# Optimization experiments

Hardware: AMD Instinct MI355X
Metric: run time of the kernel (lower is better)

Reference implementation:

```python
import jax, jax.numpy as jnp
import numpy as np

NG = 64  # number of graphs in the batch (global_add_pool output rows)

def _bn(x, g, b):
    # BatchNorm1d, training-mode batch statistics over dim 0
    mu = x.mean(0)
    var = x.var(0)
    return (x - mu) * jax.lax.rsqrt(var + 1e-5) * g + b

def _ln(x, g, b):
    mu = x.mean(-1, keepdims=True)
    var = x.var(-1, keepdims=True)
    return (x - mu) * jax.lax.rsqrt(var + 1e-5) * g + b

def _gine(x, ei, ea, eps, w1, b1, w2, b2, n):
    # GINEConv: mlp((1+eps)*x + sum_dst ReLU(x[src] + ea))
    msg = jax.nn.relu(x[ei[0]] + ea)
    agg = jax.ops.segment_sum(msg, ei[1], num_segments=n)
    h = (1.0 + eps) * x + agg
    return jax.nn.relu(h @ w1 + b1) @ w2 + b2

def setup_inputs() -> dict:
    key = jax.random.key(0)
    H, L, RW = 128, 4, 16
    Nn, m, kk = 4096, 2, 32
    S = Nn * m; SK = S * kk
    Ei, Eg = 1048576, 65536
    Vatom, Vbond = 128, 16
    ks = jax.random.split(key, 24)
    f = lambda i, shape: jax.random.normal(ks[i], shape, jnp.float32) * 0.02
    # intra edges sampled within each subgraph block to honor locality
    subs = jax.random.randint(ks[11], (Ei,), 0, S)
    src = subs * kk + jax.random.randint(ks[12], (Ei,), 0, kk)
    dst = subs * kk + jax.random.randint(ks[13], (Ei,), 0, kk)
    inp = {
        "atom_emb": f(0, (Vatom, H)), "bond_emb": f(1, (Vbond, H)),
        "rwse_w": f(2, (RW, H)), "rwse_b": jnp.zeros((H,), jnp.float32),
        "rwse": jax.random.uniform(ks[3], (Nn, RW), jnp.float32),
        "l_eps": jnp.zeros((L,), jnp.float32),
        "l_w1": f(4, (L, H, H)), "l_b1": jnp.zeros((L, H), jnp.float32),
        "l_w2": f(5, (L, H, H)), "l_b2": jnp.zeros((L, H), jnp.float32),
        "l_bng": jnp.ones((L, H), jnp.float32), "l_bnb": jnp.zeros((L, H), jnp.float32),
        "g_eps": jnp.zeros((L,), jnp.float32),
        "g_w1": f(6, (L, H, H)), "g_b1": jnp.zeros((L, H), jnp.float32),
        "g_w2": f(7, (L, H, H)), "g_b2": jnp.zeros((L, H), jnp.float32),
        "g_bng": jnp.ones((L, H), jnp.float32), "g_bnb": jnp.zeros((L, H), jnp.float32),
        "bcast_w": f(8, (L, H, H)),
        "cat_w1": f(9, (L, 2 * H, H)), "cat_b1": jnp.zeros((L, H), jnp.float32),
        "cat_w2": f(10, (L, H, H)), "cat_b2": jnp.zeros((L, H), jnp.float32),
        "ln_g": jnp.ones((L, H), jnp.float32), "ln_b": jnp.zeros((L, H), jnp.float32),
        "x_ids": jax.random.randint(ks[14], (SK,), 0, Vatom),
        "intra_ei": jnp.stack([src, dst]),
        "intra_ea_ids": jax.random.randint(ks[15], (Ei,), 0, Vbond),
        "global_ei": jax.random.randint(ks[16], (2, Eg), 0, Nn),
        "global_ea_ids": jax.random.randint(ks[17], (Eg,), 0, Vbond),
        "node_ids": jax.random.randint(ks[18], (SK,), 0, Nn),
        "valid": jax.random.randint(ks[19], (SK,), 0, 2),
        "batch": jnp.sort(jax.random.randint(ks[20], (Nn,), 0, NG)),
        "k": 32,
    }
    return inp

def reference(atom_emb, bond_emb, rwse_w, rwse_b, rwse, l_eps, l_w1, l_b1, l_w2, l_b2, l_bng, l_bnb, g_eps, g_w1, g_b1, g_w2, g_b2, g_bng, g_bnb, bcast_w, cat_w1, cat_b1, cat_w2, cat_b2, ln_g, ln_b, x_ids, intra_ei, intra_ea_ids, global_ei, global_ea_ids, node_ids, valid, batch, k):
    SK = x_ids.shape[0]; Nn = rwse.shape[0]
    S = SK // k; m = S // Nn
    H = atom_emb.shape[1]; L = l_eps.shape[0]
    ea_flat = bond_emb[intra_ea_ids]          # [Ei, H]
    g_ea = bond_emb[global_ea_ids]            # [Eg, H]
    valid_f = valid.astype(jnp.float32)[:, None]
    h = (atom_emb[x_ids] + jax.nn.relu(rwse @ rwse_w + rwse_b)[node_ids]) * valid_f  # [SK, H]
    node_assign = jnp.repeat(jnp.arange(Nn), m)   # [S]
    root_idx = jnp.arange(S) * k                  # subgraph roots in flat layout
    for i in range(L):
        h_in = h
        h_local = _bn(jax.nn.relu(_gine(h, intra_ei, ea_flat, l_eps[i], l_w1[i], l_b1[i], l_w2[i], l_b2[i], SK)), l_bng[i], l_bnb[i])
        # scatter-mean of root reps onto original nodes (each node has exactly m subgraphs)
        h_node = jax.ops.segment_sum(h[root_idx], node_assign, num_segments=Nn) / m
        h_cross = _bn(jax.nn.relu(_gine(h_node, global_ei, g_ea, g_eps[i], g_w1[i], g_b1[i], g_w2[i], g_b2[i], Nn)), g_bng[i], g_bnb[i])
        h_node = h_node + h_cross
        # broadcast projected node reps back to every flat subgraph position
        h_b = jnp.repeat((h_node @ bcast_w[i])[node_assign], k, axis=0)  # [SK, H]
        h_cat = jnp.concatenate([h_local, h_b], axis=-1)
        h_new = _ln(jax.nn.gelu(h_cat @ cat_w1[i] + cat_b1[i], approximate=False) @ cat_w2[i] + cat_b2[i], ln_g[i], ln_b[i])
        h = (h_in + h_new) * valid_f
    # per-subgraph masked mean (h is already zero at invalid rows)
    cnt = valid_f.reshape(S, k, 1).sum(1)
    h_sub = h.reshape(S, k, H).sum(1) / jnp.maximum(cnt, 1.0)   # [S, H]
    h_nodef = h_sub.reshape(Nn, m, H).mean(1)                   # [Nn, H]
    return jax.ops.segment_sum(h_nodef, batch, num_segments=NG) # [NG, H]
```

## Files before the change

kernel.cpp:

```cpp
#include <hip/hip_runtime.h>
#include <hip/hip_bf16.h>

#define H 128
#define HH 16384
#define LNUM 4
#define NN 4096
#define SS 8192
#define SKK 262144
#define EI 1048576
#define EG 65536
#define NGRAPH 64

typedef unsigned short u16;
typedef unsigned int u32;
typedef __attribute__((ext_vector_type(8))) short s16x8;
typedef __attribute__((ext_vector_type(4))) float f32x4;

__device__ __forceinline__ float b2f(u32 u){ return __uint_as_float(u<<16); }
__device__ __forceinline__ u16 f2b(float f){
  union { __hip_bfloat16 b; u16 u; } x;
  x.b=__float2bfloat16(f);
  return x.u;
}
__device__ __forceinline__ void unp8(uint4 v, float* f){
  f[0]=b2f(v.x&0xFFFF); f[1]=b2f(v.x>>16);
  f[2]=b2f(v.y&0xFFFF); f[3]=b2f(v.y>>16);
  f[4]=b2f(v.z&0xFFFF); f[5]=b2f(v.z>>16);
  f[6]=b2f(v.w&0xFFFF); f[7]=b2f(v.w>>16);
}
__device__ __forceinline__ void unp4(uint2 v, float* f){
  f[0]=b2f(v.x&0xFFFF); f[1]=b2f(v.x>>16);
  f[2]=b2f(v.y&0xFFFF); f[3]=b2f(v.y>>16);
}
__device__ __forceinline__ uint4 pk8(const float* f){
  uint4 r;
  r.x=(u32)f2b(f[0])|((u32)f2b(f[1])<<16);
  r.y=(u32)f2b(f[2])|((u32)f2b(f[3])<<16);
  r.z=(u32)f2b(f[4])|((u32)f2b(f[5])<<16);
  r.w=(u32)f2b(f[6])|((u32)f2b(f[7])<<16);
  return r;
}
__device__ __forceinline__ uint2 pk4(const float* f){
  uint2 r;
  r.x=(u32)f2b(f[0])|((u32)f2b(f[1])<<16);
  r.y=(u32)f2b(f[2])|((u32)f2b(f[3])<<16);
  return r;
}

struct CvtArgs {
  const void* p[26];
  int start[27];
};
struct TransArgs { int src[28]; };

__global__ void k_sniff(const u16* __restrict__ a, int* __restrict__ flag){
  __shared__ int cnt;
  if(threadIdx.x==0) cnt=0;
  __syncthreads();
  int big=0;
  for(int i=threadIdx.x;i<2048;i+=256){
    int e=(a[i]>>7)&0xFF;
    if(e>=127) big++;
  }
  atomicAdd(&cnt,big);
  __syncthreads();
  if(threadIdx.x==0) *flag=(cnt<16)?1:0;
}

__global__ void k_convert(CvtArgs args, const int* __restrict__ flag, float* __restrict__ dst){
  int fl=*flag;
  int total=args.start[26];
  for(int i=blockIdx.x*blockDim.x+threadIdx.x;i<total;i+=gridDim.x*blockDim.x){
    int a=0;
    while(args.start[a+1]<=i) a++;
    int j=i-args.start[a];
    float v;
    if(fl) v=b2f(((const u16*)args.p[a])[j]);
    else   v=((const float*)args.p[a])[j];
    dst[i]=v;
  }
}

__global__ __launch_bounds__(256) void k_trans(const float* __restrict__ par, TransArgs ta, u16* __restrict__ wt){
  const float* s=par+ta.src[blockIdx.x];
  u16* d=wt+(size_t)blockIdx.x*HH;
  for(int i=threadIdx.x;i<HH;i+=256){
    int j=i&7, lane=(i>>3)&63, fc=i>>9;
    int n=fc>>2, kc=fc&3, lr=lane&15, lk=lane>>4;
    int outc=n*16+lr, k=kc*32+lk*8+j;
    d[i]=f2b(s[(size_t)k*H+outc]);
  }
}

__global__ void k_cvtbond(const float* __restrict__ b, u16* __restrict__ bb){
  int i=blockIdx.x*blockDim.x+threadIdx.x;
  if(i<16*H) bb[i]=f2b(b[i]);
}

__global__ __launch_bounds__(128) void k_prepw3(const float* __restrict__ w, const float* __restrict__ cb1,
                        const float* __restrict__ stl, const float* __restrict__ gl, const float* __restrict__ bl,
                        u16* __restrict__ wt3p, float* __restrict__ bias3){
  __shared__ float red[128];
  int c=blockIdx.x, k=threadIdx.x;
  float mu=stl[k]*(1.f/262144.f);
  float var=stl[128+k]*(1.f/262144.f)-mu*mu;
  float s=gl[k]*rsqrtf(var+1e-5f);
  float tt=bl[k]-mu*s;
  float wv=w[(size_t)k*H+c];
  int idx=(((c>>4)*4+(k>>5))*64+((k>>3)&3)*16+(c&15))*8+(k&7);
  wt3p[idx]=f2b(s*wv);
  red[k]=tt*wv;
  __syncthreads();
  for(int d=64;d>0;d>>=1){ if(k<d) red[k]+=red[k+d]; __syncthreads(); }
  if(k==0) bias3[c]=cb1[c]+red[0];
}

__global__ void k_hist(const int* __restrict__ idx, int n, int shift, int* __restrict__ cnt){
  for(int i=blockIdx.x*blockDim.x+threadIdx.x;i<n;i+=gridDim.x*blockDim.x)
    atomicAdd(&cnt[idx[i]>>shift],1);
}

__global__ void k_scan(const int* __restrict__ cnt, int* __restrict__ off, int nbins){
  __shared__ int ts[1024];
  int t=threadIdx.x;
  int per=nbins>>10;
  int base=t*per;
  int s=0;
  for(int j=0;j<per;j++) s+=cnt[base+j];
  ts[t]=s;
  __syncthreads();
  for(int d=1;d<1024;d<<=1){
    int v=(t>=d)?ts[t-d]:0;
    __syncthreads();
    ts[t]+=v;
    __syncthreads();
  }
  int ex=(t==0)?0:ts[t-1];
  for(int j=0;j<per;j++){ off[base+j]=ex; ex+=cnt[base+j]; }
}

__global__ void k_scatter_i(const int* __restrict__ ei, const int* __restrict__ ea,
                            const int* __restrict__ off, int* __restrict__ cur, int* __restrict__ pack){
  for(int i=blockIdx.x*blockDim.x+threadIdx.x;i<EI;i+=gridDim.x*blockDim.x){
    int s=ei[i], d=ei[EI+i];
    int sub=d>>5;
    int pos=off[sub]+atomicAdd(&cur[sub],1);
    pack[pos]=((s&31)<<9)|((d&31)<<4)|(ea[i]&15);
  }
}

__global__ __launch_bounds__(128) void k_sortsub(const int* __restrict__ eoff, const int* __restrict__ ecnt,
                                                 int* __restrict__ epack, int* __restrict__ dstoff){
  __shared__ int ein[512];
  __shared__ int eout[512];
  __shared__ int bcnt[32];
  __shared__ int bpos[32];
  int sub=blockIdx.x, t=threadIdx.x;
  int o=eoff[sub];
  int n=ecnt[sub]; if(n>512) n=512;
  for(int i=t;i<n;i+=128) ein[i]=epack[o+i];
  if(t<32) bcnt[t]=0;
  __syncthreads();
  for(int i=t;i<n;i+=128) atomicAdd(&bcnt[(ein[i]>>4)&31],1);
  __syncthreads();
  if(t==0){
    int s=0;
    for(int b=0;b<32;b++){ bpos[b]=s; s+=bcnt[b]; }
  }
  __syncthreads();
  if(t<32) dstoff[sub*32+t]=bpos[t];
  __syncthreads();
  for(int i=t;i<n;i+=128){
    int p=ein[i];
    int pos=atomicAdd(&bpos[(p>>4)&31],1);
    eout[pos]=p;
  }
  __syncthreads();
  for(int i=t;i<n;i+=128) epack[o+i]=eout[i];
}

__global__ void k_scatter_g(const int* __restrict__ ei, const int* __restrict__ ea,
                            const int* __restrict__ off, int* __restrict__ cur, int* __restrict__ pack){
  for(int i=blockIdx.x*blockDim.x+threadIdx.x;i<EG;i+=gridDim.x*blockDim.x){
    int s=ei[i], d=ei[EG+i];
    int pos=off[d]+atomicAdd(&cur[d],1);
    pack[pos]=(s<<4)|(ea[i]&15);
  }
}

__global__ __launch_bounds__(128) void k_rwse(const float* __restrict__ rwse, const float* __restrict__ w,
                      const float* __restrict__ b, float* __restrict__ rf){
  __shared__ float ws[16*128];
  __shared__ float rv[16];
  int n=blockIdx.x, c=threadIdx.x;
  for(int i=c;i<2048;i+=128) ws[i]=w[i];
  if(c<16) rv[c]=rwse[n*16+c];
  __syncthreads();
  float acc=b[c];
  for(int j=0;j<16;j++) acc=fmaf(rv[j],ws[j*128+c],acc);
  rf[(size_t)n*H+c]=fmaxf(acc,0.f);
}

__global__ void k_h0(const float* __restrict__ atom, const float* __restrict__ rf,
                     const int* __restrict__ xids, const int* __restrict__ nids,
                     const int* __restrict__ valid, u16* __restrict__ h){
  int i=blockIdx.x*blockDim.x+threadIdx.x;
  if(i>=SKK*16) return;
  int r=i>>4, q=i&15;
  const float4* ap=(const float4*)(atom+(size_t)xids[r]*H)+q*2;
  const float4* bp=(const float4*)(rf+(size_t)nids[r]*H)+q*2;
  float4 a0=ap[0],a1=ap[1],b0=bp[0],b1=bp[1];
  float vm=valid[r]?1.f:0.f;
  float f[8]={(a0.x+b0.x)*vm,(a0.y+b0.y)*vm,(a0.z+b0.z)*vm,(a0.w+b0.w)*vm,
              (a1.x+b1.x)*vm,(a1.y+b1.y)*vm,(a1.z+b1.z)*vm,(a1.w+b1.w)*vm};
  ((uint4*)h)[i]=pk8(f);
}

template<int TAIL>
__global__ __launch_bounds__(256,4) void k_fused1(
    const u16* __restrict__ h, const u16* __restrict__ beb,
    const int* __restrict__ eoff, const int* __restrict__ ecnt, const int* __restrict__ epack,
    const int* __restrict__ dstoff,
    const float* __restrict__ epsp, int layer,
    const u16* __restrict__ W1p, const float* __restrict__ b1,
    const u16* __restrict__ W2p, const float* __restrict__ b2,
    u16* __restrict__ Xg, float* __restrict__ stats,
    const u16* __restrict__ W3p, const float* __restrict__ bias3,
    const u16* __restrict__ bbv,
    const u16* __restrict__ Wc2p, const float* __restrict__ cb2,
    const float* __restrict__ lng, const float* __restrict__ lnb,
    const int* __restrict__ validv, u16* __restrict__ hio)
{
  __shared__ u16 hs[64*128];
  __shared__ u16 agx[64*128];
  __shared__ u16 bes[16*128];
  __shared__ u16 epku[2][512];
  __shared__ int doff[2][32];
  float* sst=(float*)&epku[0][0];

  int t=threadIdx.x;
  int grp=t>>7, c=t&127;
  size_t hbase=(size_t)blockIdx.x*64*H;
  int wave=t>>6, lane=t&63, lr=lane&15, lk=lane>>4;
  int rl=wave*16+lr;
  u32 rsw=((u32)(rl&7))<<4;
  int row0=blockIdx.x*64;

  {
    u32 row=(u32)(t>>4), colb=(u32)((t&15)*16);
    *(uint4*)((char*)bes+row*256+(colb^((row&7)<<4)))=((const uint4*)beb)[t];
  }
  int sub=blockIdx.x*2+grp;
  int n=min(ecnt[sub],512);
  int o=eoff[sub];
  if(c<32) doff[grp][c]=dstoff[sub*32+c];
  for(int i=c;i<n;i+=128) epku[grp][i]=(u16)epack[o+i];

  if(TAIL){
    f32x4 a1t[8];
    #pragma unroll
    for(int n8=0;n8<8;n8++) a1t[n8]=(f32x4){0.f,0.f,0.f,0.f};
    const s16x8* B0=(const s16x8*)(Xg+(size_t)(row0+rl)*H);
    #pragma unroll
    for(int kc=0;kc<4;kc++){
      s16x8 bf=B0[kc*4+lk];
      #pragma unroll
      for(int n8=0;n8<8;n8++){
        s16x8 af=*(const s16x8*)(W3p+((n8*4+kc)<<9)+lane*8);
        a1t[n8]=__builtin_amdgcn_mfma_f32_16x16x32_bf16(af,bf,a1t[n8],0,0,0);
      }
    }
    #pragma unroll
    for(int n8=0;n8<8;n8++){
      int c0=n8*16+lk*4;
      float4 b4=*(const float4*)(bias3+c0);
      float rb[4];
      unp4(*(const uint2*)(bbv+(size_t)blockIdx.x*H+c0),rb);
      float vb[4]={b4.x,b4.y,b4.z,b4.w};
      float v[4];
      #pragma unroll
      for(int j=0;j<4;j++){
        float x=a1t[n8][j]+vb[j]+rb[j];
        v[j]=0.5f*x*(1.f+erff(x*0.70710678118654752f));
      }
      *(uint2*)((char*)agx+(u32)rl*256+(((u32)(2*c0))^rsw))=pk4(v);
    }
    f32x4 a2t[8];
    #pragma unroll
    for(int n8=0;n8<8;n8++) a2t[n8]=(f32x4){0.f,0.f,0.f,0.f};
    #pragma unroll
    for(int kc=0;kc<4;kc++){
      u32 cb=(u32)((kc*32+lk*8)*2);
      s16x8 bf=*(const s16x8*)((char*)agx+(u32)rl*256+(cb^rsw));
      #pragma unroll
      for(int n8=0;n8<8;n8++){
        s16x8 af=*(const s16x8*)(Wc2p+((n8*4+kc)<<9)+lane*8);
        a2t[n8]=__builtin_amdgcn_mfma_f32_16x16x32_bf16(af,bf,a2t[n8],0,0,0);
      }
    }
    {
      float s=0.f,q=0.f;
      #pragma unroll
      for(int n8=0;n8<8;n8++){
        int c0=n8*16+lk*4;
        float4 b4=*(const float4*)(cb2+c0);
        float vb[4]={b4.x,b4.y,b4.z,b4.w};
        #pragma unroll
        for(int j=0;j<4;j++){
          float v=a2t[n8][j]+vb[j];
          a2t[n8][j]=v;
          s+=v; q+=v*v;
        }
      }
      s+=__shfl_xor(s,16); s+=__shfl_xor(s,32);
      q+=__shfl_xor(q,16); q+=__shfl_xor(q,32);
      float mu=s*(1.f/128.f);
      float rsig=rsqrtf(q*(1.f/128.f)-mu*mu+1e-5f);
      #pragma unroll
      for(int n8=0;n8<8;n8++){
        int c0=n8*16+lk*4;
        float4 g4=*(const float4*)(lng+c0);
        float4 e4=*(const float4*)(lnb+c0);
        float g[4]={g4.x,g4.y,g4.z,g4.w}, e[4]={e4.x,e4.y,e4.z,e4.w};
        float ov[4];
        #pragma unroll
        for(int j=0;j<4;j++) ov[j]=(a2t[n8][j]-mu)*rsig*g[j]+e[j];
        *(uint2*)((char*)agx+(u32)rl*256+(((u32)(2*c0))^rsw))=pk4(ov);
      }
    }
    __syncthreads();
    uint4* hp=(uint4*)(hio+hbase);
    #pragma unroll
    for(int p=0;p<4;p++){
      int i=t+p*256;
      u32 row=(u32)(i>>4), colb=(u32)((i&15)*16);
      int grow=row0+(int)row;
      uint4 v=*(const uint4*)((const char*)agx+row*256+(colb^((row&7)<<4)));
      uint4 r=hp[i];
      float vv[8],rv[8],o8[8];
      unp8(v,vv); unp8(r,rv);
      float vm=validv[grow]?1.f:0.f;
      #pragma unroll
      for(int j=0;j<8;j++) o8[j]=(rv[j]+vv[j])*vm;
      uint4 pk=pk8(o8);
      hp[i]=pk;
      *(uint4*)((char*)hs+row*256+(colb^((row&7)<<4)))=pk;
    }
  } else {
    const uint4* src=(const uint4*)(h+hbase);
    #pragma unroll
    for(int i0=0;i0<4;i0++){
      int i=t+i0*256;
      u32 row=(u32)(i>>4), colb=(u32)((i&15)*16);
      *(uint4*)((char*)hs+row*256+(colb^((row&7)<<4)))=src[i];
    }
  }
  __syncthreads();

  {
    float ep=1.f+epsp[layer];
    #pragma unroll
    for(int p=0;p<4;p++){
      int i=t+p*256;
      u32 row=(u32)(i>>4), colb=(u32)((i&15)*16);
      u32 off=row*256+(colb^((row&7)<<4));
      float hf[8],o8[8];
      unp8(*(const uint4*)((const char*)hs+off),hf);
      #pragma unroll
      for(int j=0;j<8;j++) o8[j]=ep*hf[j];
      *(uint4*)((char*)agx+off)=pk8(o8);
    }
  }
  __syncthreads();

  {
    int slot=c>>4, chg=c&15;
    u32 cbyte=(u32)chg*16;
    int d0=slot*4;
    int sA=doff[grp][d0],   eAs=doff[grp][d0+1];
    int sB=doff[grp][d0+1], eBs=doff[grp][d0+2];
    int sC=doff[grp][d0+2], eCs=doff[grp][d0+3];
    int sD=doff[grp][d0+3];
    int eDs=(d0+3==31)?n:doff[grp][d0+4];
    int c1=eAs-sA;
    int c2=c1+eBs-sB;
    int c3=c2+eCs-sC;
    int tot=c3+eDs-sD;
    const u16* ep_=&epku[grp][0];
    auto VIDX=[&](int j)->int{
      return (j<c1)? sA+j : (j<c2)? sB+j-c1 : (j<c3)? sC+j-c2 : sD+j-c3;
    };
    auto LDP=[&](int p, uint4& hv, uint4& bv){
      u32 srow=(u32)(grp*32+(p>>9));
      u32 erow=(u32)(p&15);
      hv=*(const uint4*)((const char*)hs+srow*256+(cbyte^((srow&7)<<4)));
      bv=*(const uint4*)((const char*)bes+erow*256+(cbyte^((erow&7)<<4)));
    };
    int pA=0,pBv=0,pP0=0,pP1=0;
    uint4 hvA,bvA,hvB,bvB;
    hvA=bvA=hvB=bvB=make_uint4(0,0,0,0);
    if(tot>0){ pA=ep_[VIDX(0)]; LDP(pA,hvA,bvA); }
    if(tot>1){ pBv=ep_[VIDX(1)]; LDP(pBv,hvB,bvB); }
    pP0=(tot>2)?ep_[VIDX(2)]:0;
    pP1=(tot>3)?ep_[VIDX(3)]:0;
    float acc[8]={0.f,0.f,0.f,0.f,0.f,0.f,0.f,0.f};
    int cur=-1;
    int j=0;
    while(j<tot){
      {
        float hf[8],bf8[8];
        unp8(hvA,hf); unp8(bvA,bf8);
        int pc=pA;
        if(j+2<tot){ pA=pP0; LDP(pA,hvA,bvA); }
        pP0=pP1;
        pP1=ep_[(j+4<tot)?VIDX(j+4):0];
        int dl=(pc>>4)&31;
        if(dl!=cur){
          if(cur>=0){
            u32 drow=(u32)(grp*32+cur);
            u32 aoff=drow*256+(cbyte^((drow&7)<<4));
            float of[8];
            unp8(*(const uint4*)((const char*)agx+aoff),of);
            #pragma unroll
            for(int q=0;q<8;q++) of[q]+=acc[q];
            *(uint4*)((char*)agx+aoff)=pk8(of);
          }
          #pragma unroll
          for(int q=0;q<8;q++) acc[q]=0.f;
          cur=dl;
        }
        #pragma unroll
        for(int q=0;q<8;q++) acc[q]+=fmaxf(hf[q]+bf8[q],0.f);
      }
      j++;
      if(j>=tot) break;
      {
        float hf[8],bf8[8];
        unp8(hvB,hf); unp8(bvB,bf8);
        int pc=pBv;
        if(j+2<tot){ pBv=pP0; LDP(pBv,hvB,bvB); }
        pP0=pP1;
        pP1=ep_[(j+4<tot)?VIDX(j+4):0];
        int dl=(pc>>4)&31;
        if(dl!=cur){
          if(cur>=0){
            u32 drow=(u32)(grp*32+cur);
            u32 aoff=drow*256+(cbyte^((drow&7)<<4));
            float of[8];
            unp8(*(const uint4*)((const char*)agx+aoff),of);
            #pragma unroll
            for(int q=0;q<8;q++) of[q]+=acc[q];
            *(uint4*)((char*)agx+aoff)=pk8(of);
          }
          #pragma unroll
          for(int q=0;q<8;q++) acc[q]=0.f;
          cur=dl;
        }
        #pragma unroll
        for(int q=0;q<8;q++) acc[q]+=fmaxf(hf[q]+bf8[q],0.f);
      }
      j++;
    }
    if(cur>=0){
      u32 drow=(u32)(grp*32+cur);
      u32 aoff=drow*256+(cbyte^((drow&7)<<4));
      float of[8];
      unp8(*(const uint4*)((const char*)agx+aoff),of);
      #pragma unroll
      for(int q=0;q<8;q++) of[q]+=acc[q];
      *(uint4*)((char*)agx+aoff)=pk8(of);
    }
  }
  __syncthreads();
  sst[t]=0.f;
  __syncthreads();

  f32x4 a1[8];
  #pragma unroll
  for(int n8=0;n8<8;n8++) a1[n8]=(f32x4){0.f,0.f,0.f,0.f};
  #pragma unroll
  for(int kc=0;kc<4;kc++){
    u32 cb=(u32)((kc*32+lk*8)*2);
    s16x8 bf=*(const s16x8*)((char*)agx+(u32)rl*256+(cb^rsw));
    #pragma unroll
    for(int n8=0;n8<8;n8++){
      s16x8 af=*(const s16x8*)(W1p+((n8*4+kc)<<9)+lane*8);
      a1[n8]=__builtin_amdgcn_mfma_f32_16x16x32_bf16(af,bf,a1[n8],0,0,0);
    }
  }
  #pragma unroll
  for(int n8=0;n8<8;n8++){
    int c0=n8*16+lk*4;
    float4 b4=*(const float4*)(b1+c0);
    float v[4]={fmaxf(a1[n8][0]+b4.x,0.f),fmaxf(a1[n8][1]+b4.y,0.f),
                fmaxf(a1[n8][2]+b4.z,0.f),fmaxf(a1[n8][3]+b4.w,0.f)};
    *(uint2*)((char*)hs+(u32)rl*256+(((u32)(2*c0))^rsw))=pk4(v);
  }
  f32x4 a2[8];
  #pragma unroll
  for(int n8=0;n8<8;n8++) a2[n8]=(f32x4){0.f,0.f,0.f,0.f};
  #pragma unroll
  for(int kc=0;kc<4;kc++){
    u32 cb=(u32)((kc*32+lk*8)*2);
    s16x8 bf=*(const s16x8*)((char*)hs+(u32)rl*256+(cb^rsw));
    #pragma unroll
    for(int n8=0;n8<8;n8++){
      s16x8 af=*(const s16x8*)(W2p+((n8*4+kc)<<9)+lane*8);
      a2[n8]=__builtin_amdgcn_mfma_f32_16x16x32_bf16(af,bf,a2[n8],0,0,0);
    }
  }
  #pragma unroll
  for(int n8=0;n8<8;n8++){
    int c0=n8*16+lk*4;
    float4 b4=*(const float4*)(b2+c0);
    float v[4]={fmaxf(a2[n8][0]+b4.x,0.f),fmaxf(a2[n8][1]+b4.y,0.f),
                fmaxf(a2[n8][2]+b4.z,0.f),fmaxf(a2[n8][3]+b4.w,0.f)};
    *(uint2*)((char*)agx+(u32)rl*256+(((u32)(2*c0))^rsw))=pk4(v);
    float s[4],q[4];
    #pragma unroll
    for(int j2=0;j2<4;j2++){ s[j2]=v[j2]; q[j2]=v[j2]*v[j2]; }
    #pragma unroll
    for(int j2=0;j2<4;j2++){
      #pragma unroll
      for(int d=1;d<16;d<<=1){
        s[j2]+=__shfl_xor(s[j2],d);
        q[j2]+=__shfl_xor(q[j2],d);
      }
    }
    if(lr==0){
      #pragma unroll
      for(int j2=0;j2<4;j2++){
        atomicAdd(&sst[c0+j2],s[j2]);
        atomicAdd(&sst[128+c0+j2],q[j2]);
      }
    }
  }
  __syncthreads();
  uint4* out4=(uint4*)(Xg+hbase);
  #pragma unroll
  for(int p=0;p<4;p++){
    int i=t+p*256;
    u32 row=(u32)(i>>4), colb=(u32)((i&15)*16);
    out4[i]=*(const uint4*)((const char*)agx+row*256+(colb^((row&7)<<4)));
  }
  atomicAdd(&stats[t],sst[t]);
}

__global__ __launch_bounds__(256) void k_mlp2n(
    const u16* __restrict__ A, const u16* __restrict__ W1p, const float* __restrict__ b1,
    const u16* __restrict__ W2p, const float* __restrict__ b2,
    u16* __restrict__ out, float* __restrict__ stats)
{
  __shared__ u16 T[64*128];
  __shared__ float sst[256];
  int t=threadIdx.x;
  sst[t]=0.f;
  int wave=t>>6, lane=t&63, lr=lane&15, lk=lane>>4;
  int rl=wave*16+lr;
  u32 rsw=((u32)(rl&7))<<4;
  int row0=blockIdx.x*64;
  f32x4 a1[8];
  #pragma unroll
  for(int n8=0;n8<8;n8++) a1[n8]=(f32x4){0.f,0.f,0.f,0.f};
  const s16x8* B0=(const s16x8*)(A+(size_t)(row0+rl)*H);
  #pragma unroll
  for(int kc=0;kc<4;kc++){
    s16x8 bf=B0[kc*4+lk];
    #pragma unroll
    for(int n8=0;n8<8;n8++){
      s16x8 af=*(const s16x8*)(W1p+((n8*4+kc)<<9)+lane*8);
      a1[n8]=__builtin_amdgcn_mfma_f32_16x16x32_bf16(af,bf,a1[n8],0,0,0);
    }
  }
  #pragma unroll
  for(int n8=0;n8<8;n8++){
    int c0=n8*16+lk*4;
    float4 b4=*(const float4*)(b1+c0);
    float v[4]={fmaxf(a1[n8][0]+b4.x,0.f),fmaxf(a1[n8][1]+b4.y,0.f),
                fmaxf(a1[n8][2]+b4.z,0.f),fmaxf(a1[n8][3]+b4.w,0.f)};
    *(uint2*)((char*)T+(u32)rl*256+(((u32)(2*c0))^rsw))=pk4(v);
  }
  f32x4 a2[8];
  #pragma unroll
  for(int n8=0;n8<8;n8++) a2[n8]=(f32x4){0.f,0.f,0.f,0.f};
  #pragma unroll
  for(int kc=0;kc<4;kc++){
    u32 cb=(u32)((kc*32+lk*8)*2);
    s16x8 bf=*(const s16x8*)((char*)T+(u32)rl*256+(cb^rsw));
    #pragma unroll
    for(int n8=0;n8<8;n8++){
      s16x8 af=*(const s16x8*)(W2p+((n8*4+kc)<<9)+lane*8);
      a2[n8]=__builtin_amdgcn_mfma_f32_16x16x32_bf16(af,bf,a2[n8],0,0,0);
    }
  }
  #pragma unroll
  for(int n8=0;n8<8;n8++){
    int c0=n8*16+lk*4;
    float4 b4=*(const float4*)(b2+c0);
    float v[4]={fmaxf(a2[n8][0]+b4.x,0.f),fmaxf(a2[n8][1]+b4.y,0.f),
                fmaxf(a2[n8][2]+b4.z,0.f),fmaxf(a2[n8][3]+b4.w,0.f)};
    *(uint2*)((char*)T+(u32)rl*256+(((u32)(2*c0))^rsw))=pk4(v);
    float s[4],q[4];
    #pragma unroll
    for(int j=0;j<4;j++){ s[j]=v[j]; q[j]=v[j]*v[j]; }
    #pragma unroll
    for(int j=0;j<4;j++){
      #pragma unroll
      for(int d=1;d<16;d<<=1){
        s[j]+=__shfl_xor(s[j],d);
        q[j]+=__shfl_xor(q[j],d);
      }
    }
    if(lr==0){
      #pragma unroll
      for(int j=0;j<4;j++){
        atomicAdd(&sst[c0+j],s[j]);
        atomicAdd(&sst[128+c0+j],q[j]);
      }
    }
  }
  __syncthreads();
  uint4* out4=(uint4*)(out+(size_t)row0*H);
  #pragma unroll
  for(int p=0;p<4;p++){
    int i=t+p*256;
    u32 row=(u32)(i>>4), colb=(u32)((i&15)*16);
    out4[i]=*(const uint4*)((const char*)T+row*256+(colb^((row&7)<<4)));
  }
  atomicAdd(&stats[t],sst[t]);
}

__global__ __launch_bounds__(256) void k_bcast(
    const u16* __restrict__ hn, const u16* __restrict__ ag,
    const float* __restrict__ stg, const float* __restrict__ gg, const float* __restrict__ bg,
    const u16* __restrict__ Wbcp, const u16* __restrict__ Wc1p,
    u16* __restrict__ bb)
{
  __shared__ u16 T[64*128];
  __shared__ u16 T2[64*128];
  __shared__ float ssh[128], tsh[128];
  int t=threadIdx.x;
  int row0=blockIdx.x*64;
  if(t<128){
    float mu=stg[t]*(1.f/4096.f);
    float var=stg[128+t]*(1.f/4096.f)-mu*mu;
    float s=gg[t]*rsqrtf(var+1e-5f);
    ssh[t]=s; tsh[t]=bg[t]-mu*s;
  }
  __syncthreads();
  #pragma unroll
  for(int i0=0;i0<4;i0++){
    int i=t+i0*256;
    u32 row=(u32)(i>>4);
    int cb8=(i&15)*8;
    float hv[8],av[8],o8[8];
    unp8(((const uint4*)(hn+(size_t)row0*H))[i],hv);
    unp8(((const uint4*)(ag+(size_t)row0*H))[i],av);
    #pragma unroll
    for(int j=0;j<8;j++) o8[j]=hv[j]+fmaf(av[j],ssh[cb8+j],tsh[cb8+j]);
    *(uint4*)((char*)T+row*256+(((u32)(cb8*2))^((row&7)<<4)))=pk8(o8);
  }
  __syncthreads();
  int wave=t>>6, lane=t&63, lr=lane&15, lk=lane>>4;
  int rl=wave*16+lr;
  u32 rsw=((u32)(rl&7))<<4;
  f32x4 a1[8];
  #pragma unroll
  for(int n8=0;n8<8;n8++) a1[n8]=(f32x4){0.f,0.f,0.f,0.f};
  #pragma unroll
  for(int kc=0;kc<4;kc++){
    u32 cb=(u32)((kc*32+lk*8)*2);
    s16x8 bf=*(const s16x8*)((char*)T+(u32)rl*256+(cb^rsw));
    #pragma unroll
    for(int n8=0;n8<8;n8++){
      s16x8 af=*(const s16x8*)(Wbcp+((n8*4+kc)<<9)+lane*8);
      a1[n8]=__builtin_amdgcn_mfma_f32_16x16x32_bf16(af,bf,a1[n8],0,0,0);
    }
  }
  #pragma unroll
  for(int n8=0;n8<8;n8++){
    int c0=n8*16+lk*4;
    float v[4]={a1[n8][0],a1[n8][1],a1[n8][2],a1[n8][3]};
    *(uint2*)((char*)T2+(u32)rl*256+(((u32)(2*c0))^rsw))=pk4(v);
  }
  f32x4 a2[8];
  #pragma unroll
  for(int n8=0;n8<8;n8++) a2[n8]=(f32x4){0.f,0.f,0.f,0.f};
  #pragma unroll
  for(int kc=0;kc<4;kc++){
    u32 cb=(u32)((kc*32+lk*8)*2);
    s16x8 bf=*(const s16x8*)((char*)T2+(u32)rl*256+(cb^rsw));
    #pragma unroll
    for(int n8=0;n8<8;n8++){
      s16x8 af=*(const s16x8*)(Wc1p+((n8*4+kc)<<9)+lane*8);
      a2[n8]=__builtin_amdgcn_mfma_f32_16x16x32_bf16(af,bf,a2[n8],0,0,0);
    }
  }
  #pragma unroll
  for(int n8=0;n8<8;n8++){
    int c0=n8*16+lk*4;
    float v[4]={a2[n8][0],a2[n8][1],a2[n8][2],a2[n8][3]};
    *(uint2*)((char*)T+(u32)rl*256+(((u32)(2*c0))^rsw))=pk4(v);
  }
  __syncthreads();
  uint4* out4=(uint4*)(bb+(size_t)row0*H);
  #pragma unroll
  for(int p=0;p<4;p++){
    int i=t+p*256;
    u32 row=(u32)(i>>4), colb=(u32)((i&15)*16);
    out4[i]=*(const uint4*)((const char*)T+row*256+(colb^((row&7)<<4)));
  }
}

__global__ __launch_bounds__(256) void k_tailpool(
    const u16* __restrict__ X, const u16* __restrict__ W3p, const float* __restrict__ bias3,
    const u16* __restrict__ bb,
    const u16* __restrict__ W2p, const float* __restrict__ cb2,
    const float* __restrict__ lng, const float* __restrict__ lnb,
    const int* __restrict__ validv, const u16* __restrict__ hres,
    const int* __restrict__ batch, float* __restrict__ oacc)
{
  __shared__ u16 T[64*128];
  __shared__ float pbuf[256];
  __shared__ float cntsh[2];
  int t=threadIdx.x;
  int wave=t>>6, lane=t&63, lr=lane&15, lk=lane>>4;
  int rl=wave*16+lr;
  u32 rsw=((u32)(rl&7))<<4;
  int row0=blockIdx.x*64;
  f32x4 acc[8];
  #pragma unroll
  for(int n8=0;n8<8;n8++) acc[n8]=(f32x4){0.f,0.f,0.f,0.f};
  const s16x8* B0=(const s16x8*)(X+(size_t)(row0+rl)*H);
  #pragma unroll
  for(int kc=0;kc<4;kc++){
    s16x8 bf=B0[kc*4+lk];
    #pragma unroll
    for(int n8=0;n8<8;n8++){
      s16x8 af=*(const s16x8*)(W3p+((n8*4+kc)<<9)+lane*8);
      acc[n8]=__builtin_amdgcn_mfma_f32_16x16x32_bf16(af,bf,acc[n8],0,0,0);
    }
  }
  #pragma unroll
  for(int n8=0;n8<8;n8++){
    int c0=n8*16+lk*4;
    float4 b4=*(const float4*)(bias3+c0);
    float rb[4];
    unp4(*(const uint2*)(bb+(size_t)blockIdx.x*H+c0),rb);
    float vb[4]={b4.x,b4.y,b4.z,b4.w};
    float v[4];
    #pragma unroll
    for(int j=0;j<4;j++){
      float x=acc[n8][j]+vb[j]+rb[j];
      v[j]=0.5f*x*(1.f+erff(x*0.70710678118654752f));
    }
    *(uint2*)((char*)T+(u32)rl*256+(((u32)(2*c0))^rsw))=pk4(v);
  }
  f32x4 a2[8];
  #pragma unroll
  for(int n8=0;n8<8;n8++) a2[n8]=(f32x4){0.f,0.f,0.f,0.f};
  #pragma unroll
  for(int kc=0;kc<4;kc++){
    u32 cb=(u32)((kc*32+lk*8)*2);
    s16x8 bf=*(const s16x8*)((char*)T+(u32)rl*256+(cb^rsw));
    #pragma unroll
    for(int n8=0;n8<8;n8++){
      s16x8 af=*(const s16x8*)(W2p+((n8*4+kc)<<9)+lane*8);
      a2[n8]=__builtin_amdgcn_mfma_f32_16x16x32_bf16(af,bf,a2[n8],0,0,0);
    }
  }
  {
    float s=0.f,q=0.f;
    #pragma unroll
    for(int n8=0;n8<8;n8++){
      int c0=n8*16+lk*4;
      float4 b4=*(const float4*)(cb2+c0);
      float vb[4]={b4.x,b4.y,b4.z,b4.w};
      #pragma unroll
      for(int j=0;j<4;j++){
        float v=a2[n8][j]+vb[j];
        a2[n8][j]=v;
        s+=v; q+=v*v;
      }
    }
    s+=__shfl_xor(s,16); s+=__shfl_xor(s,32);
    q+=__shfl_xor(q,16); q+=__shfl_xor(q,32);
    float mu=s*(1.f/128.f);
    float rsig=rsqrtf(q*(1.f/128.f)-mu*mu+1e-5f);
    #pragma unroll
    for(int n8=0;n8<8;n8++){
      int c0=n8*16+lk*4;
      float4 g4=*(const float4*)(lng+c0);
      float4 e4=*(const float4*)(lnb+c0);
      float g[4]={g4.x,g4.y,g4.z,g4.w}, e[4]={e4.x,e4.y,e4.z,e4.w};
      float ov[4];
      #pragma unroll
      for(int j=0;j<4;j++) ov[j]=(a2[n8][j]-mu)*rsig*g[j]+e[j];
      *(uint2*)((char*)T+(u32)rl*256+(((u32)(2*c0))^rsw))=pk4(ov);
    }
  }
  pbuf[t]=0.f;
  if(t<2){
    int s=0;
    for(int j2=0;j2<32;j2++) s+=validv[row0+t*32+j2]?1:0;
    cntsh[t]=fmaxf((float)s,1.f);
  }
  __syncthreads();
  const uint4* hp=(const uint4*)(hres+(size_t)row0*H);
  float s0[8]={0,0,0,0,0,0,0,0}, s1[8]={0,0,0,0,0,0,0,0};
  #pragma unroll
  for(int p=0;p<4;p++){
    int i=t+p*256;
    u32 row=(u32)(i>>4), colb=(u32)((i&15)*16);
    int grow=row0+(int)row;
    uint4 v=*(const uint4*)((const char*)T+row*256+(colb^((row&7)<<4)));
    uint4 r=hp[i];
    float vv[8],rv[8];
    unp8(v,vv); unp8(r,rv);
    float vm=validv[grow]?1.f:0.f;
    #pragma unroll
    for(int j2=0;j2<8;j2++){
      float hn=(rv[j2]+vv[j2])*vm;
      if(p<2) s0[j2]+=hn; else s1[j2]+=hn;
    }
  }
  #pragma unroll
  for(int j2=0;j2<8;j2++){
    s0[j2]+=__shfl_xor(s0[j2],16); s0[j2]+=__shfl_xor(s0[j2],32);
    s1[j2]+=__shfl_xor(s1[j2],16); s1[j2]+=__shfl_xor(s1[j2],32);
  }
  if((lane&48)==0){
    int ch=(lane&15)*8;
    #pragma unroll
    for(int j2=0;j2<8;j2++){
      atomicAdd(&pbuf[ch+j2],s0[j2]);
      atomicAdd(&pbuf[128+ch+j2],s1[j2]);
    }
  }
  __syncthreads();
  if(t<128){
    float nodef=0.5f*(pbuf[t]/cntsh[0]+pbuf[128+t]/cntsh[1]);
    atomicAdd(&oacc[batch[blockIdx.x]*H+t],nodef);
  }
}

__global__ void k_npool(const u16* __restrict__ h, u16* __restrict__ hn){
  int i=blockIdx.x*blockDim.x+threadIdx.x;
  if(i>=NN*16) return;
  int n=i>>4, q=i&15;
  const uint4* hp=(const uint4*)h;
  float a[8],b[8],o[8];
  unp8(hp[(size_t)n*1024+q],a);
  unp8(hp[(size_t)n*1024+512+q],b);
  #pragma unroll
  for(int e=0;e<8;e++) o[e]=(a[e]+b[e])*0.5f;
  ((uint4*)hn)[i]=pk8(o);
}

__global__ __launch_bounds__(128) void k_gagg(const u16* __restrict__ hn, const float* __restrict__ be,
                      const int* __restrict__ goff, const int* __restrict__ gcnt,
                      const int* __restrict__ gpack, const float* __restrict__ epsp, int layer,
                      u16* __restrict__ hhg){
  __shared__ float bes[16][128];
  int n=blockIdx.x, c=threadIdx.x;
  for(int i=0;i<16;i++) bes[i][c]=be[i*128+c];
  __syncthreads();
  float acc=0.f;
  int o=goff[n], e=o+gcnt[n];
  for(;o<e;o++){
    int p=gpack[o];
    acc+=fmaxf(b2f(hn[(size_t)(p>>4)*H+c])+bes[p&15][c],0.f);
  }
  hhg[(size_t)n*H+c]=f2b(fmaf(1.f+epsp[layer],b2f(hn[(size_t)n*H+c]),acc));
}

__global__ void k_out(const float* __restrict__ acc, const int* __restrict__ flag, void* __restrict__ out){
  int i=blockIdx.x*blockDim.x+threadIdx.x;
  if(i>=NGRAPH*H) return;
  if(*flag) ((__hip_bfloat16*)out)[i]=__float2bfloat16(acc[i]);
  else ((float*)out)[i]=acc[i];
}

extern "C" void kernel_launch(void* const* d_in, const int* in_sizes, int n_in,
                              void* d_out, int out_size, void* d_ws, size_t ws_size,
                              hipStream_t stream){
  (void)n_in; (void)out_size;
  int pofs[27]; pofs[0]=0;
  for(int i=0;i<26;i++) pofs[i+1]=pofs[i]+in_sizes[i];
  int ptot=pofs[26];

  char* wsb=(char*)d_ws;
  size_t off=0;
  auto alloc=[&](size_t bytes)->char*{ char* p=wsb+off; off+=(bytes+255)&~(size_t)255; return p; };
  int*   flag =(int*)  alloc(4);
  float* par  =(float*)alloc((size_t)ptot*4);
  u16*   h    =(u16*)  alloc((size_t)SKK*H*2);
  u16*   X    =(u16*)  alloc((size_t)SKK*H*2);
  u16*   wt   =(u16*)  alloc((size_t)28*HH*2);
  u16*   wt3  =(u16*)  alloc((size_t)HH*2);
  float* bias3=(float*)alloc(H*4);
  float* rf   =(float*)alloc((size_t)NN*H*4);
  u16*   bondb=(u16*)  alloc((size_t)16*H*2);
  u16*   hn   =(u16*)  alloc((size_t)NN*H*2);
  u16*   hhg  =(u16*)  alloc((size_t)NN*H*2);
  u16*   ag   =(u16*)  alloc((size_t)NN*H*2);
  u16*   bb   =(u16*)  alloc((size_t)NN*H*2);
  int*   ecnt =(int*)  alloc(SS*4);
  int*   ecur =(int*)  alloc(SS*4);
  int*   gcnt =(int*)  alloc(NN*4);
  int*   gcur =(int*)  alloc(NN*4);
  float* stats=(float*)alloc(LNUM*512*4);
  float* oacc =(float*)alloc((size_t)NGRAPH*H*4);
  size_t zbytes=(size_t)SS*4+SS*4+NN*4+NN*4+LNUM*512*4+(size_t)NGRAPH*H*4;
  int* eoff  =(int*)alloc(SS*4);
  int* epack =(int*)alloc((size_t)EI*4);
  int* dstoff=(int*)alloc((size_t)SS*32*4);
  int* goff  =(int*)alloc(NN*4);
  int* gpack =(int*)alloc((size_t)EG*4);

  if(off>ws_size) return;

  const int* xids =(const int*)d_in[26];
  const int* iei  =(const int*)d_in[27];
  const int* iea  =(const int*)d_in[28];
  const int* gei  =(const int*)d_in[29];
  const int* gea  =(const int*)d_in[30];
  const int* nids =(const int*)d_in[31];
  const int* valid=(const int*)d_in[32];
  const int* batch=(const int*)d_in[33];

  const float* atom=par+pofs[0];
  const float* bond=par+pofs[1];
  const float* rw_w=par+pofs[2];
  const float* rw_b=par+pofs[3];
  const float* rwse=par+pofs[4];
  const float* leps=par+pofs[5];
  const float* lb1 =par+pofs[7];
  const float* lb2 =par+pofs[9];
  const float* lbng=par+pofs[10];
  const float* lbnb=par+pofs[11];
  const float* geps=par+pofs[12];
  const float* gb1 =par+pofs[14];
  const float* gb2 =par+pofs[16];
  const float* gbng=par+pofs[17];
  const float* gbnb=par+pofs[18];
  const float* cw1 =par+pofs[20];
  const float* cb1 =par+pofs[21];
  const float* cb2 =par+pofs[23];
  const float* lngp=par+pofs[24];
  const float* lnbp=par+pofs[25];

  k_sniff<<<1,256,0,stream>>>((const u16*)d_in[0], flag);
  CvtArgs ca;
  for(int i=0;i<26;i++){ ca.p[i]=d_in[i]; ca.start[i]=pofs[i]; }
  ca.start[26]=ptot;
  k_convert<<<1024,256,0,stream>>>(ca, flag, par);

  TransArgs ta;
  for(int l=0;l<LNUM;l++){
    ta.src[l*7+0]=pofs[6]+l*HH;
    ta.src[l*7+1]=pofs[8]+l*HH;
    ta.src[l*7+2]=pofs[13]+l*HH;
    ta.src[l*7+3]=pofs[15]+l*HH;
    ta.src[l*7+4]=pofs[19]+l*HH;
    ta.src[l*7+5]=pofs[20]+l*2*HH+HH;
    ta.src[l*7+6]=pofs[22]+l*HH;
  }
  k_trans<<<28,256,0,stream>>>(par, ta, wt);
  k_cvtbond<<<8,256,0,stream>>>(bond, bondb);

  (void)hipMemsetAsync(ecnt,0,zbytes,stream);

  k_hist<<<2048,256,0,stream>>>(iei+EI, EI, 5, ecnt);
  k_scan<<<1,1024,0,stream>>>(ecnt, eoff, SS);
  k_scatter_i<<<2048,256,0,stream>>>(iei, iea, eoff, ecur, epack);
  k_sortsub<<<SS,128,0,stream>>>(eoff, ecnt, epack, dstoff);
  k_hist<<<512,256,0,stream>>>(gei+EG, EG, 0, gcnt);
  k_scan<<<1,1024,0,stream>>>(gcnt, goff, NN);
  k_scatter_g<<<512,256,0,stream>>>(gei, gea, goff, gcur, gpack);

  k_rwse<<<NN,128,0,stream>>>(rwse, rw_w, rw_b, rf);
  k_h0<<<(SKK*16)/256,256,0,stream>>>(atom, rf, xids, nids, valid, h);

  for(int l=0;l<LNUM;l++){
    float* stl_l=stats+l*512;
    float* stg_l=stats+l*512+256;
    if(l==0){
      k_fused1<0><<<SS/2,256,0,stream>>>(h, bondb, eoff, ecnt, epack, dstoff, leps, l,
          wt+(size_t)(l*7+0)*HH, lb1+l*H, wt+(size_t)(l*7+1)*HH, lb2+l*H, X, stl_l,
          nullptr,nullptr,nullptr,nullptr,nullptr,nullptr,nullptr,nullptr,nullptr);
    } else {
      int pl=l-1;
      k_fused1<1><<<SS/2,256,0,stream>>>(h, bondb, eoff, ecnt, epack, dstoff, leps, l,
          wt+(size_t)(l*7+0)*HH, lb1+l*H, wt+(size_t)(l*7+1)*HH, lb2+l*H, X, stl_l,
          wt3, bias3, bb, wt+(size_t)(pl*7+6)*HH, cb2+pl*H,
          lngp+pl*H, lnbp+pl*H, valid, h);
    }
    k_npool<<<(NN*16)/256,256,0,stream>>>(h, hn);
    k_gagg<<<NN,128,0,stream>>>(hn, bond, goff, gcnt, gpack, geps, l, hhg);
    k_mlp2n<<<NN/64,256,0,stream>>>(hhg, wt+(size_t)(l*7+2)*HH, gb1+l*H,
        wt+(size_t)(l*7+3)*HH, gb2+l*H, ag, stg_l);
    k_bcast<<<NN/64,256,0,stream>>>(hn, ag, stg_l, gbng+l*H, gbnb+l*H,
        wt+(size_t)(l*7+4)*HH, wt+(size_t)(l*7+5)*HH, bb);
    k_prepw3<<<128,128,0,stream>>>(cw1+(size_t)l*2*HH, cb1+l*H, stl_l, lbng+l*H, lbnb+l*H, wt3, bias3);
  }
  {
    int l=LNUM-1;
    k_tailpool<<<SKK/64,256,0,stream>>>(X, wt3, bias3, bb,
        wt+(size_t)(l*7+6)*HH, cb2+l*H, lngp+l*H, lnbp+l*H, valid, h, batch, oacc);
  }
  k_out<<<(NGRAPH*H+255)/256,256,0,stream>>>(oacc, flag, d_out);
}
```

Baseline: 1.181 ms.

## Fuse initial embedding and node pooling into fused GINE kernel, simplify edge loop

Removes the separate k_h0 kernel: layer 0 of k_fused1 (new MODE 2) gathers atom and RWSE embeddings directly, writes h to global and fills shared memory in one pass. Removes k_npool by having every k_fused1 block average its two root rows into hn, since each block covers one node's two subgraphs. The per-slot edge walk now treats the four destination ranges as one contiguous span, dropping the VIDX index mapping and the extra prefetch registers. This saves one full write and reread of h plus two kernel launches per layer. It relies on the edge ranges being contiguous and on the block-to-node layout.

```diff
diff --git a/kernel.cpp b/kernel.cpp
--- a/kernel.cpp
+++ b/kernel.cpp
@@ -201,22 +201,7 @@
   rf[(size_t)n*H+c]=fmaxf(acc,0.f);
 }
 
-__global__ void k_h0(const float* __restrict__ atom, const float* __restrict__ rf,
-                     const int* __restrict__ xids, const int* __restrict__ nids,
-                     const int* __restrict__ valid, u16* __restrict__ h){
-  int i=blockIdx.x*blockDim.x+threadIdx.x;
-  if(i>=SKK*16) return;
-  int r=i>>4, q=i&15;
-  const float4* ap=(const float4*)(atom+(size_t)xids[r]*H)+q*2;
-  const float4* bp=(const float4*)(rf+(size_t)nids[r]*H)+q*2;
-  float4 a0=ap[0],a1=ap[1],b0=bp[0],b1=bp[1];
-  float vm=valid[r]?1.f:0.f;
-  float f[8]={(a0.x+b0.x)*vm,(a0.y+b0.y)*vm,(a0.z+b0.z)*vm,(a0.w+b0.w)*vm,
-              (a1.x+b1.x)*vm,(a1.y+b1.y)*vm,(a1.z+b1.z)*vm,(a1.w+b1.w)*vm};
-  ((uint4*)h)[i]=pk8(f);
-}
-
-template<int TAIL>
+template<int MODE>
 __global__ __launch_bounds__(256,4) void k_fused1(
     const u16* __restrict__ h, const u16* __restrict__ beb,
     const int* __restrict__ eoff, const int* __restrict__ ecnt, const int* __restrict__ epack,
@@ -229,7 +214,10 @@
     const u16* __restrict__ bbv,
     const u16* __restrict__ Wc2p, const float* __restrict__ cb2,
     const float* __restrict__ lng, const float* __restrict__ lnb,
-    const int* __restrict__ validv, u16* __restrict__ hio)
+    const int* __restrict__ validv, u16* __restrict__ hio,
+    const float* __restrict__ atomp, const float* __restrict__ rfp,
+    const int* __restrict__ xids, const int* __restrict__ nids,
+    u16* __restrict__ hnOut)
 {
   __shared__ u16 hs[64*128];
   __shared__ u16 agx[64*128];
@@ -256,7 +244,7 @@
   if(c<32) doff[grp][c]=dstoff[sub*32+c];
   for(int i=c;i<n;i+=128) epku[grp][i]=(u16)epack[o+i];
 
-  if(TAIL){
+  if(MODE==1){
     f32x4 a1t[8];
     #pragma unroll
     for(int n8=0;n8<8;n8++) a1t[n8]=(f32x4){0.f,0.f,0.f,0.f};
@@ -347,16 +335,35 @@
       *(uint4*)((char*)hs+row*256+(colb^((row&7)<<4)))=pk;
     }
   } else {
-    const uint4* src=(const uint4*)(h+hbase);
-    #pragma unroll
-    for(int i0=0;i0<4;i0++){
-      int i=t+i0*256;
-      u32 row=(u32)(i>>4), colb=(u32)((i&15)*16);
-      *(uint4*)((char*)hs+row*256+(colb^((row&7)<<4)))=src[i];
-    }
-  }
-  __syncthreads();
-
+    int r=t>>2, q=t&3;
+    int grow=row0+r;
+    float vm=validv[grow]?1.f:0.f;
+    const float4* ap=(const float4*)(atomp+(size_t)xids[grow]*H)+q*8;
+    const float4* bp=(const float4*)(rfp+(size_t)nids[grow]*H)+q*8;
+    u32 rowsw=((u32)(r&7))<<4;
+    uint4* hgp=(uint4*)(hio+hbase);
+    #pragma unroll
+    for(int k=0;k<4;k++){
+      float4 a0=ap[k*2], a1=ap[k*2+1], b0=bp[k*2], b1=bp[k*2+1];
+      float f[8]={(a0.x+b0.x)*vm,(a0.y+b0.y)*vm,(a0.z+b0.z)*vm,(a0.w+b0.w)*vm,
+                  (a1.x+b1.x)*vm,(a1.y+b1.y)*vm,(a1.z+b1.z)*vm,(a1.w+b1.w)*vm};
+      uint4 pk=pk8(f);
+      u32 cb=(u32)(q*64+k*16);
+      *(uint4*)((char*)hs+(u32)r*256+(cb^rowsw))=pk;
+      hgp[r*16+q*4+k]=pk;
+    }
+  }
+  __syncthreads();
+
+  if(t<16){
+    uint4 aR=*(const uint4*)((const char*)hs+(u32)t*16);
+    uint4 bR=*(const uint4*)((const char*)hs+32*256+(u32)t*16);
+    float fa[8],fb[8],fo[8];
+    unp8(aR,fa); unp8(bR,fb);
+    #pragma unroll
+    for(int j=0;j<8;j++) fo[j]=0.5f*(fa[j]+fb[j]);
+    ((uint4*)(hnOut+(size_t)blockIdx.x*H))[t]=pk8(fo);
+  }
   {
     float ep=1.f+epsp[layer];
     #pragma unroll
@@ -377,54 +384,40 @@
     int slot=c>>4, chg=c&15;
     u32 cbyte=(u32)chg*16;
     int d0=slot*4;
-    int sA=doff[grp][d0],   eAs=doff[grp][d0+1];
-    int sB=doff[grp][d0+1], eBs=doff[grp][d0+2];
-    int sC=doff[grp][d0+2], eCs=doff[grp][d0+3];
-    int sD=doff[grp][d0+3];
-    int eDs=(d0+3==31)?n:doff[grp][d0+4];
-    int c1=eAs-sA;
-    int c2=c1+eBs-sB;
-    int c3=c2+eCs-sC;
-    int tot=c3+eDs-sD;
+    int s0=doff[grp][d0];
+    int send=(d0+3==31)?n:doff[grp][d0+4];
     const u16* ep_=&epku[grp][0];
-    auto VIDX=[&](int j)->int{
-      return (j<c1)? sA+j : (j<c2)? sB+j-c1 : (j<c3)? sC+j-c2 : sD+j-c3;
-    };
     auto LDP=[&](int p, uint4& hv, uint4& bv){
       u32 srow=(u32)(grp*32+(p>>9));
       u32 erow=(u32)(p&15);
       hv=*(const uint4*)((const char*)hs+srow*256+(cbyte^((srow&7)<<4)));
       bv=*(const uint4*)((const char*)bes+erow*256+(cbyte^((erow&7)<<4)));
     };
-    int pA=0,pBv=0,pP0=0,pP1=0;
+    auto FLUSH=[&](int cur, float* acc){
+      u32 drow=(u32)(grp*32+cur);
+      u32 aoff=drow*256+(cbyte^((drow&7)<<4));
+      float of[8];
+      unp8(*(const uint4*)((const char*)agx+aoff),of);
+      #pragma unroll
+      for(int q=0;q<8;q++) of[q]+=acc[q];
+      *(uint4*)((char*)agx+aoff)=pk8(of);
+    };
+    float acc[8]={0.f,0.f,0.f,0.f,0.f,0.f,0.f,0.f};
+    int cur=-1;
     uint4 hvA,bvA,hvB,bvB;
     hvA=bvA=hvB=bvB=make_uint4(0,0,0,0);
-    if(tot>0){ pA=ep_[VIDX(0)]; LDP(pA,hvA,bvA); }
-    if(tot>1){ pBv=ep_[VIDX(1)]; LDP(pBv,hvB,bvB); }
-    pP0=(tot>2)?ep_[VIDX(2)]:0;
-    pP1=(tot>3)?ep_[VIDX(3)]:0;
-    float acc[8]={0.f,0.f,0.f,0.f,0.f,0.f,0.f,0.f};
-    int cur=-1;
-    int j=0;
-    while(j<tot){
+    int pA=0,pB=0;
+    if(s0<send){ pA=ep_[s0]; LDP(pA,hvA,bvA); }
+    if(s0+1<send){ pB=ep_[s0+1]; LDP(pB,hvB,bvB); }
+    for(int j=s0;j<send;){
       {
         float hf[8],bf8[8];
         unp8(hvA,hf); unp8(bvA,bf8);
         int pc=pA;
-        if(j+2<tot){ pA=pP0; LDP(pA,hvA,bvA); }
-        pP0=pP1;
-        pP1=ep_[(j+4<tot)?VIDX(j+4):0];
+        if(j+2<send){ pA=ep_[j+2]; LDP(pA,hvA,bvA); }
         int dl=(pc>>4)&31;
         if(dl!=cur){
-          if(cur>=0){
-            u32 drow=(u32)(grp*32+cur);
-            u32 aoff=drow*256+(cbyte^((drow&7)<<4));
-            float of[8];
-            unp8(*(const uint4*)((const char*)agx+aoff),of);
-            #pragma unroll
-            for(int q=0;q<8;q++) of[q]+=acc[q];
-            *(uint4*)((char*)agx+aoff)=pk8(of);
-          }
+          if(cur>=0) FLUSH(cur,acc);
           #pragma unroll
           for(int q=0;q<8;q++) acc[q]=0.f;
           cur=dl;
@@ -433,25 +426,15 @@
         for(int q=0;q<8;q++) acc[q]+=fmaxf(hf[q]+bf8[q],0.f);
       }
       j++;
-      if(j>=tot) break;
+      if(j>=send) break;
       {
         float hf[8],bf8[8];
         unp8(hvB,hf); unp8(bvB,bf8);
-        int pc=pBv;
-        if(j+2<tot){ pBv=pP0; LDP(pBv,hvB,bvB); }
-        pP0=pP1;
-        pP1=ep_[(j+4<tot)?VIDX(j+4):0];
+        int pc=pB;
+        if(j+2<send){ pB=ep_[j+2]; LDP(pB,hvB,bvB); }
         int dl=(pc>>4)&31;
         if(dl!=cur){
-          if(cur>=0){
-            u32 drow=(u32)(grp*32+cur);
-            u32 aoff=drow*256+(cbyte^((drow&7)<<4));
-            float of[8];
-            unp8(*(const uint4*)((const char*)agx+aoff),of);
-            #pragma unroll
-            for(int q=0;q<8;q++) of[q]+=acc[q];
-            *(uint4*)((char*)agx+aoff)=pk8(of);
-          }
+          if(cur>=0) FLUSH(cur,acc);
           #pragma unroll
           for(int q=0;q<8;q++) acc[q]=0.f;
           cur=dl;
@@ -461,15 +444,7 @@
       }
       j++;
     }
-    if(cur>=0){
-      u32 drow=(u32)(grp*32+cur);
-      u32 aoff=drow*256+(cbyte^((drow&7)<<4));
-      float of[8];
-      unp8(*(const uint4*)((const char*)agx+aoff),of);
-      #pragma unroll
-      for(int q=0;q<8;q++) of[q]+=acc[q];
-      *(uint4*)((char*)agx+aoff)=pk8(of);
-    }
+    if(cur>=0) FLUSH(cur,acc);
   }
   __syncthreads();
   sst[t]=0.f;
@@ -710,6 +685,23 @@
     u32 row=(u32)(i>>4), colb=(u32)((i&15)*16);
     out4[i]=*(const uint4*)((const char*)T+row*256+(colb^((row&7)<<4)));
   }
+}
+
+__global__ __launch_bounds__(128) void k_gagg(const u16* __restrict__ hn, const float* __restrict__ be,
+                      const int* __restrict__ goff, const int* __restrict__ gcnt,
+                      const int* __restrict__ gpack, const float* __restrict__ epsp, int layer,
+                      u16* __restrict__ hhg){
+  __shared__ float bes[16][128];
+  int n=blockIdx.x, c=threadIdx.x;
+  for(int i=0;i<16;i++) bes[i][c]=be[i*128+c];
+  __syncthreads();
+  float acc=0.f;
+  int o=goff[n], e=o+gcnt[n];
+  for(;o<e;o++){
+    int p=gpack[o];
+    acc+=fmaxf(b2f(hn[(size_t)(p>>4)*H+c])+bes[p&15][c],0.f);
+  }
+  hhg[(size_t)n*H+c]=f2b(fmaf(1.f+epsp[layer],b2f(hn[(size_t)n*H+c]),acc));
 }
 
 __global__ __launch_bounds__(256) void k_tailpool(
@@ -842,36 +834,6 @@
     float nodef=0.5f*(pbuf[t]/cntsh[0]+pbuf[128+t]/cntsh[1]);
     atomicAdd(&oacc[batch[blockIdx.x]*H+t],nodef);
   }
-}
-
-__global__ void k_npool(const u16* __restrict__ h, u16* __restrict__ hn){
-  int i=blockIdx.x*blockDim.x+threadIdx.x;
-  if(i>=NN*16) return;
-  int n=i>>4, q=i&15;
-  const uint4* hp=(const uint4*)h;
-  float a[8],b[8],o[8];
-  unp8(hp[(size_t)n*1024+q],a);
-  unp8(hp[(size_t)n*1024+512+q],b);
-  #pragma unroll
-  for(int e=0;e<8;e++) o[e]=(a[e]+b[e])*0.5f;
-  ((uint4*)hn)[i]=pk8(o);
-}
-
-__global__ __launch_bounds__(128) void k_gagg(const u16* __restrict__ hn, const float* __restrict__ be,
-                      const int* __restrict__ goff, const int* __restrict__ gcnt,
-                      const int* __restrict__ gpack, const float* __restrict__ epsp, int layer,
-                      u16* __restrict__ hhg){
-  __shared__ float bes[16][128];
-  int n=blockIdx.x, c=threadIdx.x;
-  for(int i=0;i<16;i++) bes[i][c]=be[i*128+c];
-  __syncthreads();
-  float acc=0.f;
-  int o=goff[n], e=o+gcnt[n];
-  for(;o<e;o++){
-    int p=gpack[o];
-    acc+=fmaxf(b2f(hn[(size_t)(p>>4)*H+c])+bes[p&15][c],0.f);
-  }
-  hhg[(size_t)n*H+c]=f2b(fmaf(1.f+epsp[layer],b2f(hn[(size_t)n*H+c]),acc));
 }
 
 __global__ void k_out(const float* __restrict__ acc, const int* __restrict__ flag, void* __restrict__ out){
@@ -980,29 +942,29 @@
   k_scatter_g<<<512,256,0,stream>>>(gei, gea, goff, gcur, gpack);
 
   k_rwse<<<NN,128,0,stream>>>(rwse, rw_w, rw_b, rf);
-  k_h0<<<(SKK*16)/256,256,0,stream>>>(atom, rf, xids, nids, valid, h);
 
   for(int l=0;l<LNUM;l++){
     float* stl_l=stats+l*512;
     float* stg_l=stats+l*512+256;
     if(l==0){
-      k_fused1<0><<<SS/2,256,0,stream>>>(h, bondb, eoff, ecnt, epack, dstoff, leps, l,
+      k_fused1<2><<<SS/2,256,0,stream>>>(h, bondb, eoff, ecnt, epack, dstoff, leps, l,
           wt+(size_t)(l*7+0)*HH, lb1+l*H, wt+(size_t)(l*7+1)*HH, lb2+l*H, X, stl_l,
-          nullptr,nullptr,nullptr,nullptr,nullptr,nullptr,nullptr,nullptr,nullptr);
+          nullptr,nullptr,nullptr,nullptr,nullptr,nullptr,nullptr, valid, h,
+          atom, rf, xids, nids, hn);
     } else {
       int pl=l-1;
       k_fused1<1><<<SS/2,256,0,stream>>>(h, bondb, eoff, ecnt, epack, dstoff, leps, l,
           wt+(size_t)(l*7+0)*HH, lb1+l*H, wt+(size_t)(l*7+1)*HH, lb2+l*H, X, stl_l,
           wt3, bias3, bb, wt+(size_t)(pl*7+6)*HH, cb2+pl*H,
-          lngp+pl*H, lnbp+pl*H, valid, h);
-    }
-    k_npool<<<(NN*16)/256,256,0,stream>>>(h, hn);
+          lngp+pl*H, lnbp+pl*H, valid, h,
+          nullptr, nullptr, nullptr, nullptr, hn);
+    }
+    k_prepw3<<<128,128,0,stream>>>(cw1+(size_t)l*2*HH, cb1+l*H, stl_l, lbng+l*H, lbnb+l*H, wt3, bias3);
     k_gagg<<<NN,128,0,stream>>>(hn, bond, goff, gcnt, gpack, geps, l, hhg);
     k_mlp2n<<<NN/64,256,0,stream>>>(hhg, wt+(size_t)(l*7+2)*HH, gb1+l*H,
         wt+(size_t)(l*7+3)*HH, gb2+l*H, ag, stg_l);
     k_bcast<<<NN/64,256,0,stream>>>(hn, ag, stg_l, gbng+l*H, gbnb+l*H,
         wt+(size_t)(l*7+4)*HH, wt+(size_t)(l*7+5)*HH, bb);
-    k_prepw3<<<128,128,0,stream>>>(cw1+(size_t)l*2*HH, cb1+l*H, stl_l, lbng+l*H, lbnb+l*H, wt3, bias3);
   }
   {
     int l=LNUM-1;
```

New measurement: 1.185 ms. No clear change (+0.3%).
